# Performance work log

Measured on AMD Instinct MI355X. Metric: run time of the kernel, lower is better.

The kernel has to match this reference:

```python
import jax, jax.numpy as jnp
import numpy as np
from jax import lax

X_SIZE, Z_SIZE, H, GC, PD = 256, 64, 64, 16, 2
B, K, T = 256, 16, 50
LOG_SIG_MIN, LOG_SIG_MAX, LOG_P_MAX = -10.0, 10.0, 50.0
ZX = X_SIZE + Z_SIZE
LSTM_IN = ZX + PD


def setup_inputs() -> dict:
    key = jax.random.key(0)
    ks = jax.random.split(key, 24)
    s = lambda fan_in: 1.0 / np.sqrt(fan_in)
    u = lambda k, shape, sc: jax.random.uniform(k, shape, jnp.float32, -sc, sc)
    inp = {
        'x': jax.random.normal(ks[0], (B, X_SIZE), jnp.float32),
        'z_stacked': jax.random.normal(ks[1], (K, B, Z_SIZE), jnp.float32),
        'input_seqs': jax.random.normal(ks[2], (B, 8, 2, 2, 6), jnp.float32),
        'pred_seqs': jax.random.normal(ks[3], (B, T, 2, 2, 6), jnp.float32),
        # initial_h / initial_c linears: ZX -> H
        'Wh0': u(ks[4], (H, ZX), s(ZX)), 'bh0': u(ks[5], (H,), s(ZX)),
        'Wc0': u(ks[6], (H, ZX), s(ZX)), 'bc0': u(ks[7], (H,), s(ZX)),
        # LSTMCell: gates order i,f,g,o
        'Wih': u(ks[8], (4 * H, LSTM_IN), s(H)), 'Whh': u(ks[9], (4 * H, H), s(H)),
        'bih': u(ks[10], (4 * H,), s(H)), 'bhh': u(ks[11], (4 * H,), s(H)),
        # GMM parameter heads: H -> GC / GC*PD
        'Wpi': u(ks[12], (GC, H), s(H)), 'bpi': u(ks[13], (GC,), s(H)),
        'Wmu': u(ks[14], (GC * PD, H), s(H)), 'bmu': u(ks[15], (GC * PD,), s(H)),
        'Wls': u(ks[16], (GC * PD, H), s(H)), 'bls': u(ks[17], (GC * PD,), s(H)),
        'Wcorr': u(ks[18], (GC, H), s(H)), 'bcorr': u(ks[19], (GC,), s(H)),
        'n_z_samples': K,
    }
    return inp


def _gmm2d_log_prob(log_pis, mus, log_sigmas, corrs, value):
    # log_pis/corrs: [K,B,T,GC]; mus/log_sigmas: [K,B,T,GC*PD]; value: [B,T,PD]
    ls = jnp.clip(log_sigmas, LOG_SIG_MIN, LOG_SIG_MAX).reshape(K, B, T, GC, PD)
    mu = mus.reshape(K, B, T, GC, PD)
    dx = value[None, :, :, None, :] - mu                      # [K,B,T,GC,PD]
    zscore = dx * jnp.exp(-ls)                                # dx / sigma
    one_m_rho2 = 1.0 - corrs ** 2
    quad = (zscore[..., 0] ** 2 + zscore[..., 1] ** 2
            - 2.0 * corrs * zscore[..., 0] * zscore[..., 1])
    comp = (-jnp.log(2.0 * jnp.pi) - ls.sum(-1)
            - 0.5 * jnp.log(one_m_rho2) - 0.5 * quad / one_m_rho2)
    log_pi_n = jax.nn.log_softmax(log_pis, axis=-1)
    log_p_t = jax.nn.logsumexp(log_pi_n + comp, axis=-1)      # [K,B,T]
    return jnp.minimum(log_p_t, LOG_P_MAX)


def reference(x, z_stacked, input_seqs, pred_seqs,
              Wh0, bh0, Wc0, bc0, Wih, Whh, bih, bhh,
              Wpi, bpi, Wmu, bmu, Wls, bls, Wcorr, bcorr, n_z_samples):
    tgt_future = pred_seqs[:, :, 1, 1, 2:4]                   # [B,T,2]
    tgt_present = input_seqs[:, -1, 1, 1, 2:4]                # [B,2]
    z = z_stacked.reshape(-1, z_stacked.shape[-1])            # [K*B, z]
    zx = jnp.concatenate([z, jnp.tile(x, (n_z_samples, 1))], axis=1)  # [N, ZX]
    N = zx.shape[0]
    h0 = zx @ Wh0.T + bh0
    c0 = zx @ Wc0.T + bc0
    decode_inputs = jnp.concatenate([tgt_present[:, None, :], tgt_future[:, :T - 1, :]], axis=1)  # [B,T,2]
    inputs = jnp.concatenate([
        jnp.broadcast_to(zx[:, None, :], (N, T, ZX)),
        jnp.tile(decode_inputs, (n_z_samples, 1, 1))], axis=2)  # [N,T,ZX+2]

    def step(carry, xt):
        h, c = carry
        gates = xt @ Wih.T + bih + h @ Whh.T + bhh
        i, f, g, o = jnp.split(gates, 4, axis=-1)
        c = jax.nn.sigmoid(f) * c + jax.nn.sigmoid(i) * jnp.tanh(g)
        h = jax.nn.sigmoid(o) * jnp.tanh(c)
        return (h, c), h

    _, hs = lax.scan(step, (h0, c0), jnp.swapaxes(inputs, 0, 1))  # [T,N,H]
    hs = jnp.swapaxes(hs, 0, 1)                                   # [N,T,H]

    log_pis = (hs @ Wpi.T + bpi).reshape(K, B, T, GC)
    mus = (hs @ Wmu.T + bmu).reshape(K, B, T, GC * PD)
    log_sigmas = (hs @ Wls.T + bls).reshape(K, B, T, GC * PD)
    corrs = jnp.tanh(hs @ Wcorr.T + bcorr).reshape(K, B, T, GC)

    log_p_yt_xz = _gmm2d_log_prob(log_pis, mus, log_sigmas, corrs, tgt_future)
    return log_p_yt_xz.sum(axis=2)                                # [K,B]
```

## Files before the change

kernel.cpp:

```cpp
#include <hip/hip_runtime.h>


#define T_ 50

typedef __attribute__((ext_vector_type(8))) short short8;
typedef __attribute__((ext_vector_type(4))) float f32x4;

#define MFMA(a, b, c) __builtin_amdgcn_mfma_f32_16x16x32_bf16(a, b, c, 0, 0, 0)

#define HBYTES 26214400
#define WIH_B 0
#define WH0_B 20480
#define WC0_B 25600
#define WHH_B 30720
#define PRJ_B 34816

__device__ __forceinline__ float sigf(float x)  { return 1.0f / (1.0f + __expf(-x)); }
__device__ __forceinline__ float tanh_(float x) { return 1.0f - 2.0f / (__expf(2.0f * x) + 1.0f); }

__device__ __forceinline__ void splitf(float f, unsigned short& hi, unsigned short& lo) {
    unsigned b = __float_as_uint(f);
    hi = (unsigned short)(b >> 16);
    float fh = __uint_as_float(b & 0xffff0000u);
    lo = (unsigned short)(__float_as_uint(f - fh) >> 16);
}

__device__ __forceinline__ void pack8(const float* p, short8& hi, short8& lo) {
    #pragma unroll
    for (int e = 0; e < 8; ++e) {
        unsigned short h, l;
        splitf(p[e], h, l);
        hi[e] = (short)h; lo[e] = (short)l;
    }
}

__global__ void pack_kernel(const float* __restrict__ Wih, const float* __restrict__ Whh,
                            const float* __restrict__ Wh0, const float* __restrict__ Wc0,
                            const float* __restrict__ Wpi, const float* __restrict__ Wmu,
                            const float* __restrict__ Wls, const float* __restrict__ Wcorr,
                            short8* __restrict__ WF)
{
    int id = blockIdx.x * 256 + threadIdx.x;
    if (id >= 18176) return;
    const float* src;
    int dst0, dst1;
    if (id < 10240) {
        int ks = id >> 10, rem = id & 1023;
        int q = rem >> 8, rem2 = rem & 255;
        int w = rem2 >> 6, l = rem2 & 63;
        int g = l >> 4, c = l & 15;
        src = Wih + (q*64 + w*16 + c)*322 + ks*32 + g*8;
        dst0 = WIH_B + (((ks*4 + q)*2 + 0)*4 + w)*64 + l;
        dst1 = WIH_B + (((ks*4 + q)*2 + 1)*4 + w)*64 + l;
    } else if (id < 12800) {
        int t2 = id - 10240;
        int ks = t2 >> 8, rem = t2 & 255;
        int w = rem >> 6, l = rem & 63;
        int g = l >> 4, c = l & 15;
        src = Wh0 + (w*16 + c)*320 + ks*32 + g*8;
        dst0 = WH0_B + ((ks*2 + 0)*4 + w)*64 + l;
        dst1 = WH0_B + ((ks*2 + 1)*4 + w)*64 + l;
    } else if (id < 15360) {
        int t2 = id - 12800;
        int ks = t2 >> 8, rem = t2 & 255;
        int w = rem >> 6, l = rem & 63;
        int g = l >> 4, c = l & 15;
        src = Wc0 + (w*16 + c)*320 + ks*32 + g*8;
        dst0 = WC0_B + ((ks*2 + 0)*4 + w)*64 + l;
        dst1 = WC0_B + ((ks*2 + 1)*4 + w)*64 + l;
    } else if (id < 17408) {
        int t3 = id - 15360;
        int q = t3 >> 9, rem = t3 & 511;
        int ks = rem >> 8, rem2 = rem & 255;
        int w = rem2 >> 6, l = rem2 & 63;
        int g = l >> 4, c = l & 15;
        src = Whh + (q*64 + w*16 + c)*64 + ks*32 + g*8;
        dst0 = WHH_B + (((q*2 + ks)*2 + 0)*4 + w)*64 + l;
        dst1 = WHH_B + (((q*2 + ks)*2 + 1)*4 + w)*64 + l;
    } else {
        int t4 = id - 17408;
        int pt = t4 >> 7, rem = t4 & 127;
        int ks = rem >> 6, l = rem & 63;
        int g = l >> 4, c = l & 15;
        int r3 = pt*16 + c;
        const float* p;
        if      (r3 < 16) p = Wpi   + r3*64;
        else if (r3 < 48) p = Wmu   + (r3-16)*64;
        else if (r3 < 80) p = Wls   + (r3-48)*64;
        else              p = Wcorr + (r3-80)*64;
        src = p + ks*32 + g*8;
        dst0 = PRJ_B + ((pt*2 + ks)*2 + 0)*64 + l;
        dst1 = PRJ_B + ((pt*2 + ks)*2 + 1)*64 + l;
    }
    short8 hi, lo;
    pack8(src, hi, lo);
    WF[dst0] = hi;
    WF[dst1] = lo;
}

__launch_bounds__(256, 2)
__global__ void lstm_kernel(
    const float* __restrict__ x,        const float* __restrict__ z,
    const float* __restrict__ inp_seqs, const float* __restrict__ pred_seqs,
    const float* __restrict__ Wih,      const float* __restrict__ bh0,
    const float* __restrict__ bc0,      const float* __restrict__ bih,
    const float* __restrict__ bhh,
    unsigned short* __restrict__ Hout,  const short8* __restrict__ WF)
{
    __shared__ __align__(16) float smem[4560];
    float* ZXL = smem;
    unsigned short* HB = (unsigned short*)(smem + 2592);
    unsigned short* H0h = HB;
    unsigned short* H0l = HB + 576;
    unsigned short* H1h = HB + 1152;
    unsigned short* H1l = HB + 1728;
    float* FUT = smem + 3744;
    float* PRS = smem + 4544;

    const int j = threadIdx.x;
    const int w = j >> 6;
    const int l = j & 63;
    const int g = l >> 4;
    const int c = l & 15;
    const int U = w*16 + c;
    const int blk = blockIdx.x;

    for (int e = j; e < 8*320; e += 256) {
        int s = e / 320, k = e - s*320;
        int n = blk*8 + s, kk = n >> 8, b = n & 255;
        ZXL[s*324 + k] = (k < 64) ? z[(kk*256 + b)*64 + k] : x[b*256 + (k - 64)];
    }
    for (int e = j; e < T_*16; e += 256) {
        int t = e >> 4, s = (e >> 1) & 7;
        int b = (blk*8 + s) & 255;
        FUT[e] = pred_seqs[b*1200 + t*24 + 20 + (e & 1)];
    }
    if (j < 16) {
        int b = (blk*8 + (j >> 1)) & 255;
        PRS[j] = inp_seqs[b*192 + 188 + (j & 1)];
    }
    __syncthreads();

    const int R0 = U, R1 = 64+U, R2 = 128+U, R3 = 192+U;
    f32x4 gc[4], h0a, c0a;
    {
        float b0 = bih[R0]+bhh[R0], b1 = bih[R1]+bhh[R1];
        float b2 = bih[R2]+bhh[R2], b3 = bih[R3]+bhh[R3];
        gc[0] = (f32x4){b0,b0,b0,b0}; gc[1] = (f32x4){b1,b1,b1,b1};
        gc[2] = (f32x4){b2,b2,b2,b2}; gc[3] = (f32x4){b3,b3,b3,b3};
        float bh_ = bh0[U], bc_ = bc0[U];
        h0a = (f32x4){bh_,bh_,bh_,bh_};
        c0a = (f32x4){bc_,bc_,bc_,bc_};
    }
    for (int ks = 0; ks < 10; ++ks) {
        short8 ahi, alo;
        pack8(&ZXL[(c & 7)*324 + ks*32 + g*8], ahi, alo);
        #pragma unroll
        for (int q = 0; q < 4; ++q) {
            short8 Bh = WF[WIH_B + (((ks*4 + q)*2 + 0)*4 + w)*64 + l];
            short8 Bl = WF[WIH_B + (((ks*4 + q)*2 + 1)*4 + w)*64 + l];
            gc[q] = MFMA(ahi, Bh, gc[q]);
            gc[q] = MFMA(ahi, Bl, gc[q]);
            gc[q] = MFMA(alo, Bh, gc[q]);
        }
        {
            short8 Bh = WF[WH0_B + ((ks*2 + 0)*4 + w)*64 + l];
            short8 Bl = WF[WH0_B + ((ks*2 + 1)*4 + w)*64 + l];
            h0a = MFMA(ahi, Bh, h0a); h0a = MFMA(ahi, Bl, h0a); h0a = MFMA(alo, Bh, h0a);
        }
        {
            short8 Bh = WF[WC0_B + ((ks*2 + 0)*4 + w)*64 + l];
            short8 Bl = WF[WC0_B + ((ks*2 + 1)*4 + w)*64 + l];
            c0a = MFMA(ahi, Bh, c0a); c0a = MFMA(ahi, Bl, c0a); c0a = MFMA(alo, Bh, c0a);
        }
    }

    const bool lowg = (g < 2);
    const int s0 = 4*(g & 1) + (lowg ? 0 : 2);
    float cst0 = lowg ? c0a[0] : c0a[2];
    float cst1 = lowg ? c0a[1] : c0a[3];
    {
        float hv0 = lowg ? h0a[0] : h0a[2];
        float hv1 = lowg ? h0a[1] : h0a[3];
        unsigned short hh, ll;
        splitf(hv0, hh, ll); H0h[s0*72 + U] = hh; H0l[s0*72 + U] = ll;
        splitf(hv1, hh, ll); H0h[(s0+1)*72 + U] = hh; H0l[(s0+1)*72 + U] = ll;
    }

    float wd0[4], wd1[4];
    wd0[0] = Wih[R0*322+320]; wd1[0] = Wih[R0*322+321];
    wd0[1] = Wih[R1*322+320]; wd1[1] = Wih[R1*322+321];
    wd0[2] = Wih[R2*322+320]; wd1[2] = Wih[R2*322+321];
    wd0[3] = Wih[R3*322+320]; wd1[3] = Wih[R3*322+321];
    short8 WB[4][2][2];
    #pragma unroll
    for (int q = 0; q < 4; ++q)
        #pragma unroll
        for (int ks = 0; ks < 2; ++ks)
            #pragma unroll
            for (int p = 0; p < 2; ++p)
                WB[q][ks][p] = WF[WHH_B + (((q*2 + ks)*2 + p)*4 + w)*64 + l];

    __syncthreads();

    const int nbase = blk*8;
    for (int t = 0; t < T_; ++t) {
        const unsigned short* Hh = (t & 1) ? H1h : H0h;
        const unsigned short* Hl = (t & 1) ? H1l : H0l;
        unsigned short* Nh = (t & 1) ? H0h : H1h;
        unsigned short* Nl = (t & 1) ? H0l : H1l;

        short8 ah0 = *reinterpret_cast<const short8*>(Hh + (c & 7)*72 + g*8);
        short8 al0 = *reinterpret_cast<const short8*>(Hl + (c & 7)*72 + g*8);
        short8 ah1 = *reinterpret_cast<const short8*>(Hh + (c & 7)*72 + 32 + g*8);
        short8 al1 = *reinterpret_cast<const short8*>(Hl + (c & 7)*72 + 32 + g*8);

        const float* dptr = (t == 0) ? PRS : (FUT + (t-1)*16);
        float2 dvr[4];
        #pragma unroll
        for (int r = 0; r < 4; ++r)
            dvr[r] = *reinterpret_cast<const float2*>(dptr + ((4*g + r) & 7)*2);

        f32x4 aq[4];
        #pragma unroll
        for (int q = 0; q < 4; ++q) {
            #pragma unroll
            for (int r = 0; r < 4; ++r)
                aq[q][r] = gc[q][r] + dvr[r].x*wd0[q] + dvr[r].y*wd1[q];
            aq[q] = MFMA(ah0, WB[q][0][0], aq[q]);
            aq[q] = MFMA(ah0, WB[q][0][1], aq[q]);
            aq[q] = MFMA(al0, WB[q][0][0], aq[q]);
            aq[q] = MFMA(ah1, WB[q][1][0], aq[q]);
            aq[q] = MFMA(ah1, WB[q][1][1], aq[q]);
            aq[q] = MFMA(al1, WB[q][1][0], aq[q]);
        }

        float i0 = lowg ? aq[0][0] : aq[0][2], i1 = lowg ? aq[0][1] : aq[0][3];
        float f0 = lowg ? aq[1][0] : aq[1][2], f1 = lowg ? aq[1][1] : aq[1][3];
        float g0 = lowg ? aq[2][0] : aq[2][2], g1 = lowg ? aq[2][1] : aq[2][3];
        float o0 = lowg ? aq[3][0] : aq[3][2], o1 = lowg ? aq[3][1] : aq[3][3];
        float cc0 = sigf(f0)*cst0 + sigf(i0)*tanh_(g0); cst0 = cc0;
        float cc1 = sigf(f1)*cst1 + sigf(i1)*tanh_(g1); cst1 = cc1;
        float hv0 = sigf(o0)*tanh_(cc0);
        float hv1 = sigf(o1)*tanh_(cc1);

        unsigned short hh0, ll0, hh1, ll1;
        splitf(hv0, hh0, ll0);
        splitf(hv1, hh1, ll1);
        Hout[(size_t)(t*4096 + nbase + s0)*64 + U]     = hh0;
        Hout[(size_t)(t*4096 + nbase + s0 + 1)*64 + U] = hh1;
        Nh[s0*72 + U] = hh0;  Nl[s0*72 + U] = ll0;
        Nh[(s0+1)*72 + U] = hh1;  Nl[(s0+1)*72 + U] = ll1;
        __syncthreads();
    }
}

__launch_bounds__(256, 3)
__global__ void head_kernel(const float* __restrict__ pred_seqs,
                            const float* __restrict__ bpi, const float* __restrict__ bmu,
                            const float* __restrict__ bls, const float* __restrict__ bcorr,
                            const unsigned short* __restrict__ Hin,
                            const short8* __restrict__ WF,
                            float* __restrict__ out)
{
    __shared__ __align__(16) float PL[4][1600];
    const int j = threadIdx.x;
    const int w = j >> 6;
    const int l = j & 63;
    const int g = l >> 4;
    const int c = l & 15;
    const int blk = blockIdx.x;
    const int set = blk >> 2, chunk = blk & 3;
    const int t0 = (chunk*25) >> 1, t1 = ((chunk+1)*25) >> 1;

    float bias[6];
    #pragma unroll
    for (int pt = 0; pt < 6; ++pt) {
        int r3 = pt*16 + c;
        bias[pt] = (r3 < 16) ? bpi[r3] : (r3 < 48) ? bmu[r3-16]
                 : (r3 < 80) ? bls[r3-48] : bcorr[r3-80];
    }

    const int s = l >> 2, q4 = l & 3;
    const int n_s = set*16 + s, b_s = n_s & 255;
    float* PLw = &PL[w][0];
    float sum_local = 0.0f;

    for (int t = t0 + w; t < t1; t += 4) {
        const unsigned short* hp = Hin + (size_t)(t*4096 + set*16 + c)*64;
        short8 ah0 = *reinterpret_cast<const short8*>(hp + g*8);
        short8 ah1 = *reinterpret_cast<const short8*>(hp + 32 + g*8);
        #pragma unroll
        for (int pt = 0; pt < 6; ++pt) {
            short8 B00 = WF[PRJ_B + ((pt*2 + 0)*2 + 0)*64 + l];
            short8 B01 = WF[PRJ_B + ((pt*2 + 0)*2 + 1)*64 + l];
            short8 B10 = WF[PRJ_B + ((pt*2 + 1)*2 + 0)*64 + l];
            short8 B11 = WF[PRJ_B + ((pt*2 + 1)*2 + 1)*64 + l];
            f32x4 p = (f32x4){bias[pt], bias[pt], bias[pt], bias[pt]};
            p = MFMA(ah0, B00, p);
            p = MFMA(ah0, B01, p);
            p = MFMA(ah1, B10, p);
            p = MFMA(ah1, B11, p);
            #pragma unroll
            for (int r = 0; r < 4; ++r) PLw[(4*g + r)*100 + pt*16 + c] = p[r];
        }
        asm volatile("s_waitcnt lgkmcnt(0)" ::: "memory");
        __builtin_amdgcn_sched_barrier(0);

        float2 tv = *reinterpret_cast<const float2*>(pred_seqs + b_s*1200 + t*24 + 20);
        float a[4], m = -1e30f, Ppi = 0.0f;
        #pragma unroll
        for (int i = 0; i < 4; ++i) {
            int cq = q4*4 + i;
            float pi = PLw[s*100 + cq];
            float2 mu = *reinterpret_cast<const float2*>(PLw + s*100 + 16 + 2*cq);
            float2 ls = *reinterpret_cast<const float2*>(PLw + s*100 + 48 + 2*cq);
            float co = PLw[s*100 + 80 + cq];
            float l0 = fminf(fmaxf(ls.x, -10.0f), 10.0f);
            float l1 = fminf(fmaxf(ls.y, -10.0f), 10.0f);
            float z0 = (tv.x - mu.x) * __expf(-l0);
            float z1 = (tv.y - mu.y) * __expf(-l1);
            float ct = tanh_(co);
            float omr = 1.0f - ct*ct;
            float quad = z0*z0 + z1*z1 - 2.0f*ct*z0*z1;
            float comp = -1.8378770664093453f - (l0 + l1) - 0.5f*__logf(omr) - 0.5f*quad/omr;
            a[i] = pi + comp;
            m = fmaxf(m, a[i]);
            Ppi += __expf(pi);
        }
        m = fmaxf(m, __shfl_xor(m, 1));
        m = fmaxf(m, __shfl_xor(m, 2));
        float E = __expf(a[0]-m) + __expf(a[1]-m) + __expf(a[2]-m) + __expf(a[3]-m);
        E   += __shfl_xor(E, 1);   E   += __shfl_xor(E, 2);
        Ppi += __shfl_xor(Ppi, 1); Ppi += __shfl_xor(Ppi, 2);
        float logp = m + __logf(E) - __logf(Ppi);
        sum_local += fminf(logp, 50.0f);
    }
    if (q4 == 0) atomicAdd(out + n_s, sum_local);
}

extern "C" void kernel_launch(void* const* d_in, const int* in_sizes, int n_in,
                              void* d_out, int out_size, void* d_ws, size_t ws_size,
                              hipStream_t stream) {
    const float* x     = (const float*)d_in[0];
    const float* z     = (const float*)d_in[1];
    const float* iseq  = (const float*)d_in[2];
    const float* pseq  = (const float*)d_in[3];
    const float* Wh0   = (const float*)d_in[4];
    const float* bh0   = (const float*)d_in[5];
    const float* Wc0   = (const float*)d_in[6];
    const float* bc0   = (const float*)d_in[7];
    const float* Wih   = (const float*)d_in[8];
    const float* Whh   = (const float*)d_in[9];
    const float* bih   = (const float*)d_in[10];
    const float* bhh   = (const float*)d_in[11];
    const float* Wpi   = (const float*)d_in[12];
    const float* bpi   = (const float*)d_in[13];
    const float* Wmu   = (const float*)d_in[14];
    const float* bmu   = (const float*)d_in[15];
    const float* Wls   = (const float*)d_in[16];
    const float* bls   = (const float*)d_in[17];
    const float* Wcorr = (const float*)d_in[18];
    const float* bcorr = (const float*)d_in[19];
    float* out = (float*)d_out;

    unsigned short* Hbuf = (unsigned short*)d_ws;
    short8* WF = (short8*)((char*)d_ws + HBYTES);

    pack_kernel<<<71, 256, 0, stream>>>(Wih, Whh, Wh0, Wc0, Wpi, Wmu, Wls, Wcorr, WF);
    lstm_kernel<<<512, 256, 0, stream>>>(x, z, iseq, pseq, Wih, bh0, bc0, bih, bhh,
                                         Hbuf, (const short8*)WF);
    hipMemsetAsync(d_out, 0, 4096 * sizeof(float), stream);
    head_kernel<<<1024, 256, 0, stream>>>(pseq, bpi, bmu, bls, bcorr,
                                          (const unsigned short*)Hbuf,
                                          (const short8*)WF, out);
}
```

Baseline: 114.6 us.

## Process 16 sequences per LSTM block and round Whh to single bf16

Each LSTM block now handles 16 sequences instead of 8, so every MFMA row is used and the grid shrinks from 512 to 256 blocks. The recurrent weight Whh is stored as one round-to-nearest bf16 term rather than a hi/lo split, which cuts the per-step recurrent MFMAs from 6 to 4 per gate. Decoder inputs are staged once into shared memory as a [T][16][2] table, and the per-step barrier becomes a raw s_barrier after an lgkmcnt wait. Dropping the low part of Whh lowers precision, and halving the block count may leave more of the GPU idle during the serial recurrence.

```diff
diff --git a/kernel.cpp b/kernel.cpp
--- a/kernel.cpp
+++ b/kernel.cpp
@@ -2,18 +2,17 @@
 
 
 #define T_ 50
-
 typedef __attribute__((ext_vector_type(8))) short short8;
 typedef __attribute__((ext_vector_type(4))) float f32x4;
-
-#define MFMA(a, b, c) __builtin_amdgcn_mfma_f32_16x16x32_bf16(a, b, c, 0, 0, 0)
-
-#define HBYTES 26214400
-#define WIH_B 0
-#define WH0_B 20480
-#define WC0_B 25600
-#define WHH_B 30720
-#define PRJ_B 34816
+#define MFMA(a,b,c) __builtin_amdgcn_mfma_f32_16x16x32_bf16(a,b,c,0,0,0)
+
+#define HOUT_B 0u
+#define WF_B   26214400u
+#define WIH_S 0
+#define WH0_S 320
+#define WC0_S 400
+#define WHH_S 480
+#define PRJ_S 512
 
 __device__ __forceinline__ float sigf(float x)  { return 1.0f / (1.0f + __expf(-x)); }
 __device__ __forceinline__ float tanh_(float x) { return 1.0f - 2.0f / (__expf(2.0f * x) + 1.0f); }
@@ -24,7 +23,6 @@
     float fh = __uint_as_float(b & 0xffff0000u);
     lo = (unsigned short)(__float_as_uint(f - fh) >> 16);
 }
-
 __device__ __forceinline__ void pack8(const float* p, short8& hi, short8& lo) {
     #pragma unroll
     for (int e = 0; e < 8; ++e) {
@@ -32,6 +30,15 @@
         splitf(p[e], h, l);
         hi[e] = (short)h; lo[e] = (short)l;
     }
+}
+__device__ __forceinline__ unsigned short bf16rn(float f) {
+    unsigned b = __float_as_uint(f);
+    unsigned r = b + 0x7fffu + ((b >> 16) & 1u);
+    return (unsigned short)(r >> 16);
+}
+__device__ __forceinline__ void pack8rn(const float* p, short8& hi) {
+    #pragma unroll
+    for (int e = 0; e < 8; ++e) hi[e] = (short)bf16rn(p[e]);
 }
 
 __global__ void pack_kernel(const float* __restrict__ Wih, const float* __restrict__ Whh,
@@ -42,60 +49,53 @@
 {
     int id = blockIdx.x * 256 + threadIdx.x;
     if (id >= 18176) return;
-    const float* src;
-    int dst0, dst1;
     if (id < 10240) {
         int ks = id >> 10, rem = id & 1023;
-        int q = rem >> 8, rem2 = rem & 255;
-        int w = rem2 >> 6, l = rem2 & 63;
-        int g = l >> 4, c = l & 15;
-        src = Wih + (q*64 + w*16 + c)*322 + ks*32 + g*8;
-        dst0 = WIH_B + (((ks*4 + q)*2 + 0)*4 + w)*64 + l;
-        dst1 = WIH_B + (((ks*4 + q)*2 + 1)*4 + w)*64 + l;
+        int q = rem >> 8, w = (rem >> 6) & 3, l = rem & 63;
+        int g = l >> 4, c = l & 15;
+        const float* src = Wih + (q*64 + w*16 + c)*322 + ks*32 + g*8;
+        short8 hi, lo; pack8(src, hi, lo);
+        WF[(WIH_S + ((ks*4 + q)*2 + 0)*4 + w)*64 + l] = hi;
+        WF[(WIH_S + ((ks*4 + q)*2 + 1)*4 + w)*64 + l] = lo;
     } else if (id < 12800) {
         int t2 = id - 10240;
-        int ks = t2 >> 8, rem = t2 & 255;
-        int w = rem >> 6, l = rem & 63;
-        int g = l >> 4, c = l & 15;
-        src = Wh0 + (w*16 + c)*320 + ks*32 + g*8;
-        dst0 = WH0_B + ((ks*2 + 0)*4 + w)*64 + l;
-        dst1 = WH0_B + ((ks*2 + 1)*4 + w)*64 + l;
+        int ks = t2 >> 8, w = (t2 >> 6) & 3, l = t2 & 63;
+        int g = l >> 4, c = l & 15;
+        const float* src = Wh0 + (w*16 + c)*320 + ks*32 + g*8;
+        short8 hi, lo; pack8(src, hi, lo);
+        WF[(WH0_S + (ks*2 + 0)*4 + w)*64 + l] = hi;
+        WF[(WH0_S + (ks*2 + 1)*4 + w)*64 + l] = lo;
     } else if (id < 15360) {
         int t2 = id - 12800;
-        int ks = t2 >> 8, rem = t2 & 255;
-        int w = rem >> 6, l = rem & 63;
-        int g = l >> 4, c = l & 15;
-        src = Wc0 + (w*16 + c)*320 + ks*32 + g*8;
-        dst0 = WC0_B + ((ks*2 + 0)*4 + w)*64 + l;
-        dst1 = WC0_B + ((ks*2 + 1)*4 + w)*64 + l;
+        int ks = t2 >> 8, w = (t2 >> 6) & 3, l = t2 & 63;
+        int g = l >> 4, c = l & 15;
+        const float* src = Wc0 + (w*16 + c)*320 + ks*32 + g*8;
+        short8 hi, lo; pack8(src, hi, lo);
+        WF[(WC0_S + (ks*2 + 0)*4 + w)*64 + l] = hi;
+        WF[(WC0_S + (ks*2 + 1)*4 + w)*64 + l] = lo;
     } else if (id < 17408) {
         int t3 = id - 15360;
-        int q = t3 >> 9, rem = t3 & 511;
-        int ks = rem >> 8, rem2 = rem & 255;
-        int w = rem2 >> 6, l = rem2 & 63;
-        int g = l >> 4, c = l & 15;
-        src = Whh + (q*64 + w*16 + c)*64 + ks*32 + g*8;
-        dst0 = WHH_B + (((q*2 + ks)*2 + 0)*4 + w)*64 + l;
-        dst1 = WHH_B + (((q*2 + ks)*2 + 1)*4 + w)*64 + l;
+        int slot = t3 >> 6, l = t3 & 63;
+        int g = l >> 4, c = l & 15;
+        int tile = slot >> 1, ks = slot & 1;
+        int q = tile >> 2, wt = tile & 3;
+        short8 hi; pack8rn(Whh + (q*64 + 16*wt + c)*64 + ks*32 + g*8, hi);
+        WF[(WHH_S + slot)*64 + l] = hi;
     } else {
         int t4 = id - 17408;
-        int pt = t4 >> 7, rem = t4 & 127;
-        int ks = rem >> 6, l = rem & 63;
-        int g = l >> 4, c = l & 15;
+        int r = t4 >> 6, l = t4 & 63;
+        int g = l >> 4, c = l & 15;
+        int pt = r >> 1, ks = r & 1;
         int r3 = pt*16 + c;
         const float* p;
         if      (r3 < 16) p = Wpi   + r3*64;
         else if (r3 < 48) p = Wmu   + (r3-16)*64;
         else if (r3 < 80) p = Wls   + (r3-48)*64;
         else              p = Wcorr + (r3-80)*64;
-        src = p + ks*32 + g*8;
-        dst0 = PRJ_B + ((pt*2 + ks)*2 + 0)*64 + l;
-        dst1 = PRJ_B + ((pt*2 + ks)*2 + 1)*64 + l;
-    }
-    short8 hi, lo;
-    pack8(src, hi, lo);
-    WF[dst0] = hi;
-    WF[dst1] = lo;
+        short8 hi, lo; pack8(p + ks*32 + g*8, hi, lo);
+        WF[(PRJ_S + ((pt*2 + ks)*2 + 0))*64 + l] = hi;
+        WF[(PRJ_S + ((pt*2 + ks)*2 + 1))*64 + l] = lo;
+    }
 }
 
 __launch_bounds__(256, 2)
@@ -107,151 +107,131 @@
     const float* __restrict__ bhh,
     unsigned short* __restrict__ Hout,  const short8* __restrict__ WF)
 {
-    __shared__ __align__(16) float smem[4560];
+    __shared__ __align__(16) float smem[6336];
     float* ZXL = smem;
-    unsigned short* HB = (unsigned short*)(smem + 2592);
-    unsigned short* H0h = HB;
-    unsigned short* H0l = HB + 576;
-    unsigned short* H1h = HB + 1152;
-    unsigned short* H1l = HB + 1728;
-    float* FUT = smem + 3744;
-    float* PRS = smem + 4544;
+    float* DQ  = smem;
+    unsigned short* HF0h = (unsigned short*)(smem + 5184);
+    unsigned short* HF0l = (unsigned short*)(smem + 5472);
+    unsigned short* HF1h = (unsigned short*)(smem + 5760);
+    unsigned short* HF1l = (unsigned short*)(smem + 6048);
 
     const int j = threadIdx.x;
-    const int w = j >> 6;
-    const int l = j & 63;
-    const int g = l >> 4;
-    const int c = l & 15;
-    const int U = w*16 + c;
-    const int blk = blockIdx.x;
-
-    for (int e = j; e < 8*320; e += 256) {
+    const int w = j >> 6, l = j & 63, g = l >> 4, c = l & 15;
+    const int U = 16*w + c;
+    const int blk = blockIdx.x, nb = blk*16;
+
+    for (int e = j; e < 16*320; e += 256) {
         int s = e / 320, k = e - s*320;
-        int n = blk*8 + s, kk = n >> 8, b = n & 255;
-        ZXL[s*324 + k] = (k < 64) ? z[(kk*256 + b)*64 + k] : x[b*256 + (k - 64)];
-    }
-    for (int e = j; e < T_*16; e += 256) {
-        int t = e >> 4, s = (e >> 1) & 7;
-        int b = (blk*8 + s) & 255;
-        FUT[e] = pred_seqs[b*1200 + t*24 + 20 + (e & 1)];
-    }
-    if (j < 16) {
-        int b = (blk*8 + (j >> 1)) & 255;
-        PRS[j] = inp_seqs[b*192 + 188 + (j & 1)];
+        int n = nb + s, b = n & 255;
+        ZXL[s*324 + k] = (k < 64) ? z[n*64 + k] : x[b*256 + (k - 64)];
     }
     __syncthreads();
 
-    const int R0 = U, R1 = 64+U, R2 = 128+U, R3 = 192+U;
-    f32x4 gc[4], h0a, c0a;
+    f32x4 gcA[4], h0a, c0a;
     {
-        float b0 = bih[R0]+bhh[R0], b1 = bih[R1]+bhh[R1];
-        float b2 = bih[R2]+bhh[R2], b3 = bih[R3]+bhh[R3];
-        gc[0] = (f32x4){b0,b0,b0,b0}; gc[1] = (f32x4){b1,b1,b1,b1};
-        gc[2] = (f32x4){b2,b2,b2,b2}; gc[3] = (f32x4){b3,b3,b3,b3};
+        #pragma unroll
+        for (int q = 0; q < 4; ++q) {
+            int ga = q*64 + U;
+            float b_ = bih[ga] + bhh[ga];
+            gcA[q] = (f32x4){b_, b_, b_, b_};
+        }
         float bh_ = bh0[U], bc_ = bc0[U];
-        h0a = (f32x4){bh_,bh_,bh_,bh_};
-        c0a = (f32x4){bc_,bc_,bc_,bc_};
+        h0a = (f32x4){bh_, bh_, bh_, bh_};
+        c0a = (f32x4){bc_, bc_, bc_, bc_};
     }
     for (int ks = 0; ks < 10; ++ks) {
-        short8 ahi, alo;
-        pack8(&ZXL[(c & 7)*324 + ks*32 + g*8], ahi, alo);
+        short8 ah, al;
+        pack8(&ZXL[c*324 + ks*32 + g*8], ah, al);
         #pragma unroll
         for (int q = 0; q < 4; ++q) {
-            short8 Bh = WF[WIH_B + (((ks*4 + q)*2 + 0)*4 + w)*64 + l];
-            short8 Bl = WF[WIH_B + (((ks*4 + q)*2 + 1)*4 + w)*64 + l];
-            gc[q] = MFMA(ahi, Bh, gc[q]);
-            gc[q] = MFMA(ahi, Bl, gc[q]);
-            gc[q] = MFMA(alo, Bh, gc[q]);
+            short8 Bh = WF[(WIH_S + ((ks*4 + q)*2 + 0)*4 + w)*64 + l];
+            short8 Bl = WF[(WIH_S + ((ks*4 + q)*2 + 1)*4 + w)*64 + l];
+            gcA[q] = MFMA(ah, Bh, gcA[q]);
+            gcA[q] = MFMA(ah, Bl, gcA[q]);
+            gcA[q] = MFMA(al, Bh, gcA[q]);
         }
         {
-            short8 Bh = WF[WH0_B + ((ks*2 + 0)*4 + w)*64 + l];
-            short8 Bl = WF[WH0_B + ((ks*2 + 1)*4 + w)*64 + l];
-            h0a = MFMA(ahi, Bh, h0a); h0a = MFMA(ahi, Bl, h0a); h0a = MFMA(alo, Bh, h0a);
+            short8 Bh = WF[(WH0_S + (ks*2 + 0)*4 + w)*64 + l];
+            short8 Bl = WF[(WH0_S + (ks*2 + 1)*4 + w)*64 + l];
+            h0a = MFMA(ah, Bh, h0a); h0a = MFMA(ah, Bl, h0a); h0a = MFMA(al, Bh, h0a);
         }
         {
-            short8 Bh = WF[WC0_B + ((ks*2 + 0)*4 + w)*64 + l];
-            short8 Bl = WF[WC0_B + ((ks*2 + 1)*4 + w)*64 + l];
-            c0a = MFMA(ahi, Bh, c0a); c0a = MFMA(ahi, Bl, c0a); c0a = MFMA(alo, Bh, c0a);
-        }
-    }
-
-    const bool lowg = (g < 2);
-    const int s0 = 4*(g & 1) + (lowg ? 0 : 2);
-    float cst0 = lowg ? c0a[0] : c0a[2];
-    float cst1 = lowg ? c0a[1] : c0a[3];
-    {
-        float hv0 = lowg ? h0a[0] : h0a[2];
-        float hv1 = lowg ? h0a[1] : h0a[3];
-        unsigned short hh, ll;
-        splitf(hv0, hh, ll); H0h[s0*72 + U] = hh; H0l[s0*72 + U] = ll;
-        splitf(hv1, hh, ll); H0h[(s0+1)*72 + U] = hh; H0l[(s0+1)*72 + U] = ll;
-    }
-
+            short8 Bh = WF[(WC0_S + (ks*2 + 0)*4 + w)*64 + l];
+            short8 Bl = WF[(WC0_S + (ks*2 + 1)*4 + w)*64 + l];
+            c0a = MFMA(ah, Bh, c0a); c0a = MFMA(ah, Bl, c0a); c0a = MFMA(al, Bh, c0a);
+        }
+    }
+    float cst[4];
+    #pragma unroll
+    for (int r = 0; r < 4; ++r) {
+        cst[r] = c0a[r];
+        unsigned short hh, ll; splitf(h0a[r], hh, ll);
+        HF0h[(4*g + r)*72 + U] = hh;
+        HF0l[(4*g + r)*72 + U] = ll;
+    }
     float wd0[4], wd1[4];
-    wd0[0] = Wih[R0*322+320]; wd1[0] = Wih[R0*322+321];
-    wd0[1] = Wih[R1*322+320]; wd1[1] = Wih[R1*322+321];
-    wd0[2] = Wih[R2*322+320]; wd1[2] = Wih[R2*322+321];
-    wd0[3] = Wih[R3*322+320]; wd1[3] = Wih[R3*322+321];
-    short8 WB[4][2][2];
+    #pragma unroll
+    for (int q = 0; q < 4; ++q) {
+        int ga = q*64 + U;
+        wd0[q] = Wih[ga*322 + 320];
+        wd1[q] = Wih[ga*322 + 321];
+    }
+    short8 WB[4][2];
     #pragma unroll
     for (int q = 0; q < 4; ++q)
         #pragma unroll
         for (int ks = 0; ks < 2; ++ks)
-            #pragma unroll
-            for (int p = 0; p < 2; ++p)
-                WB[q][ks][p] = WF[WHH_B + (((q*2 + ks)*2 + p)*4 + w)*64 + l];
-
+            WB[q][ks] = WF[(WHH_S + (q*4 + w)*2 + ks)*64 + l];
     __syncthreads();
 
-    const int nbase = blk*8;
+    for (int e = j; e < T_*32; e += 256) {
+        int t = e >> 5, rem = e & 31, s = rem >> 1, comp = rem & 1;
+        int b = (nb + s) & 255;
+        DQ[e] = (t == 0) ? inp_seqs[b*192 + 188 + comp]
+                         : pred_seqs[b*1200 + (t-1)*24 + 20 + comp];
+    }
+    __syncthreads();
+
     for (int t = 0; t < T_; ++t) {
-        const unsigned short* Hh = (t & 1) ? H1h : H0h;
-        const unsigned short* Hl = (t & 1) ? H1l : H0l;
-        unsigned short* Nh = (t & 1) ? H0h : H1h;
-        unsigned short* Nl = (t & 1) ? H0l : H1l;
-
-        short8 ah0 = *reinterpret_cast<const short8*>(Hh + (c & 7)*72 + g*8);
-        short8 al0 = *reinterpret_cast<const short8*>(Hl + (c & 7)*72 + g*8);
-        short8 ah1 = *reinterpret_cast<const short8*>(Hh + (c & 7)*72 + 32 + g*8);
-        short8 al1 = *reinterpret_cast<const short8*>(Hl + (c & 7)*72 + 32 + g*8);
-
-        const float* dptr = (t == 0) ? PRS : (FUT + (t-1)*16);
-        float2 dvr[4];
-        #pragma unroll
-        for (int r = 0; r < 4; ++r)
-            dvr[r] = *reinterpret_cast<const float2*>(dptr + ((4*g + r) & 7)*2);
+        const unsigned short* Hh = (t & 1) ? HF1h : HF0h;
+        const unsigned short* Hl = (t & 1) ? HF1l : HF0l;
+        unsigned short* Nh = (t & 1) ? HF0h : HF1h;
+        unsigned short* Nl = (t & 1) ? HF0l : HF1l;
+
+        short8 ah0 = *reinterpret_cast<const short8*>(Hh + c*72 +      g*8);
+        short8 al0 = *reinterpret_cast<const short8*>(Hl + c*72 +      g*8);
+        short8 ah1 = *reinterpret_cast<const short8*>(Hh + c*72 + 32 + g*8);
+        short8 al1 = *reinterpret_cast<const short8*>(Hl + c*72 + 32 + g*8);
+        f32x4 dA = *reinterpret_cast<const f32x4*>(DQ + t*32 + 8*g);
+        f32x4 dB = *reinterpret_cast<const f32x4*>(DQ + t*32 + 8*g + 4);
 
         f32x4 aq[4];
         #pragma unroll
         for (int q = 0; q < 4; ++q) {
-            #pragma unroll
-            for (int r = 0; r < 4; ++r)
-                aq[q][r] = gc[q][r] + dvr[r].x*wd0[q] + dvr[r].y*wd1[q];
-            aq[q] = MFMA(ah0, WB[q][0][0], aq[q]);
-            aq[q] = MFMA(ah0, WB[q][0][1], aq[q]);
-            aq[q] = MFMA(al0, WB[q][0][0], aq[q]);
-            aq[q] = MFMA(ah1, WB[q][1][0], aq[q]);
-            aq[q] = MFMA(ah1, WB[q][1][1], aq[q]);
-            aq[q] = MFMA(al1, WB[q][1][0], aq[q]);
-        }
-
-        float i0 = lowg ? aq[0][0] : aq[0][2], i1 = lowg ? aq[0][1] : aq[0][3];
-        float f0 = lowg ? aq[1][0] : aq[1][2], f1 = lowg ? aq[1][1] : aq[1][3];
-        float g0 = lowg ? aq[2][0] : aq[2][2], g1 = lowg ? aq[2][1] : aq[2][3];
-        float o0 = lowg ? aq[3][0] : aq[3][2], o1 = lowg ? aq[3][1] : aq[3][3];
-        float cc0 = sigf(f0)*cst0 + sigf(i0)*tanh_(g0); cst0 = cc0;
-        float cc1 = sigf(f1)*cst1 + sigf(i1)*tanh_(g1); cst1 = cc1;
-        float hv0 = sigf(o0)*tanh_(cc0);
-        float hv1 = sigf(o1)*tanh_(cc1);
-
-        unsigned short hh0, ll0, hh1, ll1;
-        splitf(hv0, hh0, ll0);
-        splitf(hv1, hh1, ll1);
-        Hout[(size_t)(t*4096 + nbase + s0)*64 + U]     = hh0;
-        Hout[(size_t)(t*4096 + nbase + s0 + 1)*64 + U] = hh1;
-        Nh[s0*72 + U] = hh0;  Nl[s0*72 + U] = ll0;
-        Nh[(s0+1)*72 + U] = hh1;  Nl[(s0+1)*72 + U] = ll1;
-        __syncthreads();
+            f32x4 a;
+            a[0] = gcA[q][0] + dA[0]*wd0[q] + dA[1]*wd1[q];
+            a[1] = gcA[q][1] + dA[2]*wd0[q] + dA[3]*wd1[q];
+            a[2] = gcA[q][2] + dB[0]*wd0[q] + dB[1]*wd1[q];
+            a[3] = gcA[q][3] + dB[2]*wd0[q] + dB[3]*wd1[q];
+            a = MFMA(ah0, WB[q][0], a);
+            a = MFMA(al0, WB[q][0], a);
+            a = MFMA(ah1, WB[q][1], a);
+            a = MFMA(al1, WB[q][1], a);
+            aq[q] = a;
+        }
+        #pragma unroll
+        for (int r = 0; r < 4; ++r) {
+            float cc = sigf(aq[1][r])*cst[r] + sigf(aq[0][r])*tanh_(aq[2][r]);
+            cst[r] = cc;
+            float hv = sigf(aq[3][r])*tanh_(cc);
+            unsigned short hh, ll; splitf(hv, hh, ll);
+            Nh[(4*g + r)*72 + U] = hh;
+            Nl[(4*g + r)*72 + U] = ll;
+            Hout[(size_t)(t*4096 + nb + 4*g + r)*64 + U] = hh;
+        }
+        asm volatile("s_waitcnt lgkmcnt(0)" ::: "memory");
+        __builtin_amdgcn_s_barrier();
+        asm volatile("" ::: "memory");
     }
 }
 
@@ -292,10 +272,10 @@
         short8 ah1 = *reinterpret_cast<const short8*>(hp + 32 + g*8);
         #pragma unroll
         for (int pt = 0; pt < 6; ++pt) {
-            short8 B00 = WF[PRJ_B + ((pt*2 + 0)*2 + 0)*64 + l];
-            short8 B01 = WF[PRJ_B + ((pt*2 + 0)*2 + 1)*64 + l];
-            short8 B10 = WF[PRJ_B + ((pt*2 + 1)*2 + 0)*64 + l];
-            short8 B11 = WF[PRJ_B + ((pt*2 + 1)*2 + 1)*64 + l];
+            short8 B00 = WF[(PRJ_S + ((pt*2 + 0)*2 + 0))*64 + l];
+            short8 B01 = WF[(PRJ_S + ((pt*2 + 0)*2 + 1))*64 + l];
+            short8 B10 = WF[(PRJ_S + ((pt*2 + 1)*2 + 0))*64 + l];
+            short8 B11 = WF[(PRJ_S + ((pt*2 + 1)*2 + 1))*64 + l];
             f32x4 p = (f32x4){bias[pt], bias[pt], bias[pt], bias[pt]};
             p = MFMA(ah0, B00, p);
             p = MFMA(ah0, B01, p);
@@ -364,14 +344,15 @@
     const float* bcorr = (const float*)d_in[19];
     float* out = (float*)d_out;
 
-    unsigned short* Hbuf = (unsigned short*)d_ws;
-    short8* WF = (short8*)((char*)d_ws + HBYTES);
+    char* ws = (char*)d_ws;
+    unsigned short* Hout = (unsigned short*)(ws + HOUT_B);
+    short8* WF = (short8*)(ws + WF_B);
 
     pack_kernel<<<71, 256, 0, stream>>>(Wih, Whh, Wh0, Wc0, Wpi, Wmu, Wls, Wcorr, WF);
-    lstm_kernel<<<512, 256, 0, stream>>>(x, z, iseq, pseq, Wih, bh0, bc0, bih, bhh,
-                                         Hbuf, (const short8*)WF);
     hipMemsetAsync(d_out, 0, 4096 * sizeof(float), stream);
+    lstm_kernel<<<256, 256, 0, stream>>>(x, z, iseq, pseq, Wih, bh0, bc0, bih, bhh,
+                                         Hout, (const short8*)WF);
     head_kernel<<<1024, 256, 0, stream>>>(pseq, bpi, bmu, bls, bcorr,
-                                          (const unsigned short*)Hbuf,
+                                          (const unsigned short*)Hout,
                                           (const short8*)WF, out);
 }
```

New measurement: 110.7 us. 1.03x faster.
